# Kernel tuning notes

Measured on AMD Instinct MI355X. Metric: run time of the kernel, lower is better.

The kernel has to match this reference:

```python
import jax, jax.numpy as jnp
import numpy as np
from jax import lax

B, S, F, H, A, C = 256, 128, 128, 512, 512, 128


def _gru_cell(x, h, Wih, Whh, bih, bhh):
    # PyTorch GRU cell: gates ordered (r, z, n)
    gi = x @ Wih.T + bih            # [B, 3H]
    gh = h @ Whh.T + bhh            # [B, 3H]
    ir, iz, inn = jnp.split(gi, 3, axis=-1)
    hr, hz, hn = jnp.split(gh, 3, axis=-1)
    r = jax.nn.sigmoid(ir + hr)
    z = jax.nn.sigmoid(iz + hz)
    n = jnp.tanh(inn + r * hn)
    return (1.0 - z) * n + z * h


def setup_inputs() -> dict:
    key = jax.random.key(0)
    ks = jax.random.split(key, 13)
    def n(k, shape, s=0.05):
        return jax.random.normal(k, shape, dtype=jnp.float32) * s
    return dict(
        x=n(ks[0], (B, S, F), 1.0),
        y=jax.random.randint(ks[1], (B, C), 0, S),
        enc_Wih=n(ks[2], (3 * H, F)), enc_Whh=n(ks[3], (3 * H, H)),
        enc_bih=n(ks[4], (3 * H,)), enc_bhh=n(ks[5], (3 * H,)),
        dec_Wih=n(ks[6], (3 * H, F)), dec_Whh=n(ks[7], (3 * H, H)),
        dec_bih=n(ks[8], (3 * H,)), dec_bhh=n(ks[9], (3 * H,)),
        w1=n(ks[10], (A, H)), w2=n(ks[11], (A, H)), v=n(ks[12], (A,)),
    )


def reference(x, y, enc_Wih, enc_Whh, enc_bih, enc_bhh,
              dec_Wih, dec_Whh, dec_bih, dec_bhh, w1, w2, v):
    b, s, f = x.shape
    c = y.shape[1]
    h0 = jnp.zeros((b, H), x.dtype)

    # ---- encoder GRU over sequence ----
    def enc_step(h, xt):
        h2 = _gru_cell(xt, h, enc_Wih, enc_Whh, enc_bih, enc_bhh)
        return h2, h2
    hT, enc_out = lax.scan(enc_step, h0, jnp.swapaxes(x, 0, 1))  # enc_out [S,B,H]
    enc_out = jnp.swapaxes(enc_out, 0, 1)                        # [B,S,H]

    # w1(enc_out) is loop-invariant: precompute (same math as recomputing per step)
    enc_proj = jnp.einsum('bsh,ah->bsa', enc_out, w1)            # [B,S,A]

    # ---- decoder pointer loop (teacher_force_ratio=0.0 -> always use argmax) ----
    def dec_step(carry, y_i):
        h, dec_in = carry
        h = _gru_cell(dec_in, h, dec_Wih, dec_Whh, dec_bih, dec_bhh)  # [B,H]
        att = jax.nn.relu(enc_proj + (h @ w2.T)[:, None, :])          # [B,S,A]
        prob = jax.nn.softmax(jnp.einsum('bsa,a->bs', att, v), axis=1)  # [B,S]
        # faithful to original: F.cross_entropy applied to probabilities
        logp = jax.nn.log_softmax(prob, axis=1)
        step_loss = -jnp.mean(jnp.take_along_axis(logp, y_i[:, None], axis=1))
        pred = jnp.argmax(prob, axis=1)                               # [B]
        dec_in_next = jnp.take_along_axis(x, pred[:, None, None], axis=1)[:, 0, :]
        return (h, dec_in_next), (pred, step_loss)

    dec_in0 = jnp.zeros((b, f), x.dtype)
    (_, _), (preds, losses) = lax.scan(dec_step, (hT, dec_in0), y.T)
    preds = preds.T                                   # [B, C]
    loss = jnp.sum(losses) / b / c
    return preds, loss
```

## Files before the change

kernel.cpp:

```cpp
#include <hip/hip_runtime.h>
#include <math.h>

#define B_ 256
#define S_ 128
#define F_ 128
#define H_ 512
#define A_ 512
#define C_ 128
#define HSLICE (H_ * B_)

#define DOT4(va, vb) ((va).x*(vb).x + (va).y*(vb).y + (va).z*(vb).z + (va).w*(vb).w)

template<int NH>
__device__ __forceinline__ void acc_chunks(const float* __restrict__ src,
                                           const float* __restrict__ W6k,
                                           int nk, int b, float* __restrict__ acc)
{
    float a0[32], a1[32];
#pragma unroll
    for (int j = 0; j < 32; ++j) a0[j] = src[(size_t)j * B_ + b];
    for (int kc = 0; kc < nk; kc += 32) {
        if (kc + 32 < nk) {
#pragma unroll
            for (int j = 0; j < 32; ++j)
                a1[j] = src[(size_t)(kc + 32 + j) * B_ + b];
        }
        const float* Wr = W6k + (size_t)kc * 6;
#pragma unroll
        for (int j = 0; j < 32; ++j) {
            float av = a0[j];
            acc[0]    = fmaf(av, Wr[j * 6 + 0], acc[0]);
            acc[1]    = fmaf(av, Wr[j * 6 + 1], acc[1]);
            acc[2]    = fmaf(av, Wr[j * 6 + 2], acc[2]);
            acc[3]    = fmaf(av, Wr[j * 6 + 3], acc[3]);
            acc[NH]   = fmaf(av, Wr[j * 6 + 4], acc[NH]);
            acc[NH+1] = fmaf(av, Wr[j * 6 + 5], acc[NH + 1]);
        }
#pragma unroll
        for (int j = 0; j < 32; ++j) a0[j] = a1[j];
    }
}

__device__ __forceinline__ void acc_xrow(const float4* __restrict__ xr,
                                         const float* __restrict__ W6k,
                                         float* __restrict__ acc)
{
    float4 c0[8], c1[8];
#pragma unroll
    for (int j = 0; j < 8; ++j) c0[j] = xr[j];
    for (int q = 0; q < 32; q += 8) {
        if (q + 8 < 32) {
#pragma unroll
            for (int j = 0; j < 8; ++j) c1[j] = xr[q + 8 + j];
        }
#pragma unroll
        for (int j = 0; j < 8; ++j) {
            const float* Wr = W6k + (size_t)((q + j) * 4) * 6;
            float e0 = c0[j].x, e1 = c0[j].y, e2 = c0[j].z, e3 = c0[j].w;
#pragma unroll
            for (int t2 = 0; t2 < 4; ++t2) {
                float av = (t2 == 0) ? e0 : (t2 == 1) ? e1 : (t2 == 2) ? e2 : e3;
                acc[0] = fmaf(av, Wr[t2 * 6 + 0], acc[0]);
                acc[1] = fmaf(av, Wr[t2 * 6 + 1], acc[1]);
                acc[2] = fmaf(av, Wr[t2 * 6 + 2], acc[2]);
                acc[3] = fmaf(av, Wr[t2 * 6 + 3], acc[3]);
                acc[4] = fmaf(av, Wr[t2 * 6 + 4], acc[4]);
                acc[5] = fmaf(av, Wr[t2 * 6 + 5], acc[5]);
            }
        }
#pragma unroll
        for (int j = 0; j < 8; ++j) c0[j] = c1[j];
    }
}

__global__ __launch_bounds__(256)
void prep_all(const float* __restrict__ x,
              const float* __restrict__ eWih, const float* __restrict__ eWhh,
              const float* __restrict__ ebih, const float* __restrict__ ebhh,
              const float* __restrict__ dbih, const float* __restrict__ dbhh,
              float* __restrict__ xT, float* __restrict__ W6e,
              float* __restrict__ bias4e, float* __restrict__ bias4d,
              float* __restrict__ h0T)
{
    int id = blockIdx.x * 256 + threadIdx.x;
    {
        int up = id / 3840;
        int rem = id - up * 3840;
        int k = rem / 6, g = rem - k * 6;
        int row = (g >> 1) * H_ + up * 2 + (g & 1);
        float val;
        if (k < F_) val = eWih[(size_t)row * F_ + k];
        else        val = eWhh[(size_t)row * H_ + (k - F_)];
        W6e[id] = val;
    }
#pragma unroll
    for (int r = 0; r < 5; ++r) {
        int xid = id + r * 983040;
        if (xid < S_ * F_ * B_) {
            int b2 = xid & 255, f = (xid >> 8) & 127, t = xid >> 15;
            xT[xid] = x[(size_t)b2 * (S_ * F_) + (size_t)t * F_ + f];
        }
    }
    if (id < H_ * B_) h0T[id] = 0.f;
    if (id < H_) {
        bias4e[id * 4 + 0] = ebih[id] + ebhh[id];
        bias4e[id * 4 + 1] = ebih[H_ + id] + ebhh[H_ + id];
        bias4e[id * 4 + 2] = ebih[2 * H_ + id];
        bias4e[id * 4 + 3] = ebhh[2 * H_ + id];
        bias4d[id * 4 + 0] = dbih[id] + dbhh[id];
        bias4d[id * 4 + 1] = dbih[H_ + id] + dbhh[H_ + id];
        bias4d[id * 4 + 2] = dbih[2 * H_ + id];
        bias4d[id * 4 + 3] = dbhh[2 * H_ + id];
    }
}

__global__ __launch_bounds__(256)
void prep_dec(const float* __restrict__ dWih, const float* __restrict__ dWhh,
              const float* __restrict__ w2,
              float* __restrict__ W6d, float4* __restrict__ w2q)
{
    int id = blockIdx.x * 256 + threadIdx.x;
    {
        int up = id / 3840;
        int rem = id - up * 3840;
        int k = rem / 6, g = rem - k * 6;
        int row = (g >> 1) * H_ + up * 2 + (g & 1);
        float val;
        if (k < F_) val = dWih[(size_t)row * F_ + k];
        else        val = dWhh[(size_t)row * H_ + (k - F_)];
        W6d[id] = val;
    }
    if (id < 128 * 512) {
        int k4 = id >> 9, a = id & 511;
        const float* s = w2 + (size_t)a * H_ + k4 * 4;
        w2q[id] = make_float4(s[0], s[1], s[2], s[3]);
    }
}

__global__ __launch_bounds__(128)
void gru_step(const float* __restrict__ inT,
              const float* __restrict__ x,
              const int*   __restrict__ pred,
              const float* __restrict__ hinT,
              const float* __restrict__ W6,
              const float* __restrict__ bias4,
              float* __restrict__ houtT,
              float* __restrict__ hB)
{
    __shared__ float accL[64][6];
    const int tid = threadIdx.x;
    const int lane = tid & 63;
    const int kw = tid >> 6;
    const int up = blockIdx.x & 255;
    const int bh = blockIdx.x >> 8;
    const int b = bh * 64 + lane;
    const float* Wb = W6 + (size_t)up * 3840;
    const int u0 = up * 2, u1 = u0 + 1;

    float acc[8];
#pragma unroll
    for (int g = 0; g < 8; ++g) acc[g] = 0.f;

    float hold0 = 0.f, hold1 = 0.f;
    if (kw == 0) {
        hold0 = hinT[(size_t)u0 * B_ + b];
        hold1 = hinT[(size_t)u1 * B_ + b];
        if (inT) {
            acc_chunks<4>(inT, Wb, F_, b, acc);
        } else if (pred) {
            int pb = pred[b];
            const float4* xr = (const float4*)(x + ((size_t)b * S_ + pb) * F_);
            acc_xrow(xr, Wb, acc);
        }
        acc_chunks<6>(hinT, Wb + F_ * 6, 192, b, acc);
    } else {
        acc_chunks<6>(hinT + (size_t)192 * B_, Wb + 320 * 6, 320, b, acc);
    }

    if (kw == 1) {
        accL[lane][0] = acc[0]; accL[lane][1] = acc[1];
        accL[lane][2] = acc[2]; accL[lane][3] = acc[3];
        accL[lane][4] = acc[6]; accL[lane][5] = acc[7];
    }
    __syncthreads();
    if (kw == 0) {
        const float4 bb0 = *(const float4*)(bias4 + u0 * 4);
        const float4 bb1 = *(const float4*)(bias4 + u1 * 4);
        float rr0 = 1.f / (1.f + expf(-(acc[0] + accL[lane][0] + bb0.x)));
        float rr1 = 1.f / (1.f + expf(-(acc[1] + accL[lane][1] + bb1.x)));
        float zz0 = 1.f / (1.f + expf(-(acc[2] + accL[lane][2] + bb0.y)));
        float zz1 = 1.f / (1.f + expf(-(acc[3] + accL[lane][3] + bb1.y)));
        float hn0 = acc[6] + accL[lane][4] + bb0.w;
        float hn1 = acc[7] + accL[lane][5] + bb1.w;
        float nn0 = tanhf(acc[4] + bb0.z + rr0 * hn0);
        float nn1 = tanhf(acc[5] + bb1.z + rr1 * hn1);
        float h0v = (1.f - zz0) * nn0 + zz0 * hold0;
        float h1v = (1.f - zz1) * nn1 + zz1 * hold1;
        houtT[(size_t)u0 * B_ + b] = h0v;
        houtT[(size_t)u1 * B_ + b] = h1v;
        if (hB) {
            hB[(size_t)b * H_ + u0] = h0v;
            hB[(size_t)b * H_ + u1] = h1v;
        }
    }
}

__global__ __launch_bounds__(512)
void w2attn_step(const float* __restrict__ hB,
                 const float4* __restrict__ w2q,
                 const float* __restrict__ v, const int* __restrict__ y,
                 int step, const float* __restrict__ proj,
                 int* __restrict__ predBuf,
                 float* __restrict__ nlogp, float* __restrict__ preds_out)
{
    const int b = blockIdx.x;
    const int tid = threadIdx.x;
    __shared__ float sh[512];
    __shared__ float sq[512];
    __shared__ float sScore[S_], sProb[S_];

    sh[tid] = hB[(size_t)b * H_ + tid];
    __syncthreads();

    {
        float acc = 0.f;
        const float4* wp = w2q + tid;
#pragma unroll 8
        for (int k4 = 0; k4 < 128; ++k4) {
            float4 hv = *(const float4*)&sh[k4 * 4];
            float4 wv4 = wp[(size_t)k4 * 512];
            acc += DOT4(hv, wv4);
        }
        sq[tid] = acc;
    }
    __syncthreads();

    const int wv = tid >> 6, ln = tid & 63;
    float4 q0 = *(const float4*)&sq[ln * 8];
    float4 q1 = *(const float4*)&sq[ln * 8 + 4];
    float4 v0r = *(const float4*)(v + ln * 8);
    float4 v1r = *(const float4*)(v + ln * 8 + 4);
    const float* epb = proj + (size_t)b * (S_ * A_);
    for (int si = 0; si < 16; ++si) {
        int s = si * 8 + wv;
        const float* row = epb + (size_t)s * A_ + ln * 8;
        float4 p0 = *(const float4*)(row);
        float4 p1 = *(const float4*)(row + 4);
        float acc = fmaxf(p0.x + q0.x, 0.f) * v0r.x
                  + fmaxf(p0.y + q0.y, 0.f) * v0r.y
                  + fmaxf(p0.z + q0.z, 0.f) * v0r.z
                  + fmaxf(p0.w + q0.w, 0.f) * v0r.w
                  + fmaxf(p1.x + q1.x, 0.f) * v1r.x
                  + fmaxf(p1.y + q1.y, 0.f) * v1r.y
                  + fmaxf(p1.z + q1.z, 0.f) * v1r.z
                  + fmaxf(p1.w + q1.w, 0.f) * v1r.w;
#pragma unroll
        for (int off = 32; off; off >>= 1) acc += __shfl_down(acc, off);
        if (ln == 0) sScore[s] = acc;
    }
    __syncthreads();

    if (tid < 64) {
        float s0v = sScore[tid], s1v = sScore[tid + 64];
        float m = fmaxf(s0v, s1v);
#pragma unroll
        for (int off = 32; off; off >>= 1) m = fmaxf(m, __shfl_xor(m, off));
        float e0 = expf(s0v - m), e1 = expf(s1v - m);
        float se = e0 + e1;
#pragma unroll
        for (int off = 32; off; off >>= 1) se += __shfl_xor(se, off);
        float p0 = e0 / se, p1 = e1 / se;
        sProb[tid] = p0; sProb[tid + 64] = p1;
        float pm = fmaxf(p0, p1);
#pragma unroll
        for (int off = 32; off; off >>= 1) pm = fmaxf(pm, __shfl_xor(pm, off));
        float t0 = expf(p0 - pm), t1 = expf(p1 - pm);
        float T = t0 + t1;
#pragma unroll
        for (int off = 32; off; off >>= 1) T += __shfl_xor(T, off);
        float bv = p0; int bi2 = tid;
        if (p1 > bv) { bv = p1; bi2 = tid + 64; }
#pragma unroll
        for (int off = 32; off; off >>= 1) {
            float ov = __shfl_xor(bv, off);
            int oi = __shfl_xor(bi2, off);
            if (ov > bv || (ov == bv && oi < bi2)) { bv = ov; bi2 = oi; }
        }
        if (tid == 0) {
            int yy = y[(size_t)b * C_ + step];
            float py = sProb[yy];
            nlogp[(size_t)step * B_ + b] = -(py - pm - logf(T));
            preds_out[(size_t)b * C_ + step] = (float)bi2;
            predBuf[b] = bi2;
        }
    }
}

__global__ __launch_bounds__(256)
void proj_gemm(const float* __restrict__ encT, const float* __restrict__ w1,
               float* __restrict__ proj)
{
    __shared__ float sA[32][128];
    __shared__ float sB[32][132];
    const int tid = threadIdx.x;
    const int s = blockIdx.z;
    const int b0 = blockIdx.y * 128;
    const int a0 = blockIdx.x * 128;
    const int tx = tid & 15, ty = tid >> 4;

    float acc[8][8];
#pragma unroll
    for (int i = 0; i < 8; ++i)
#pragma unroll
        for (int j = 0; j < 8; ++j) acc[i][j] = 0.f;

    const float* Abase = encT + (size_t)s * HSLICE + b0;
    for (int kc = 0; kc < H_; kc += 32) {
#pragma unroll
        for (int p = 0; p < 16; ++p) {
            int idx = tid + p * 256;
            int kj = idx >> 7, bbb = idx & 127;
            sA[kj][bbb] = Abase[(size_t)(kc + kj) * B_ + bbb];
        }
#pragma unroll
        for (int p = 0; p < 16; ++p) {
            int idx = tid + p * 256;
            int aa = idx >> 5, kj = idx & 31;
            sB[kj][aa] = w1[(size_t)(a0 + aa) * H_ + kc + kj];
        }
        __syncthreads();
#pragma unroll
        for (int kj = 0; kj < 32; ++kj) {
            float4 af0 = *(const float4*)&sA[kj][ty * 8];
            float4 af1 = *(const float4*)&sA[kj][ty * 8 + 4];
            float4 bf0 = *(const float4*)&sB[kj][tx * 8];
            float4 bf1 = *(const float4*)&sB[kj][tx * 8 + 4];
            float am[8] = {af0.x, af0.y, af0.z, af0.w, af1.x, af1.y, af1.z, af1.w};
            float bn[8] = {bf0.x, bf0.y, bf0.z, bf0.w, bf1.x, bf1.y, bf1.z, bf1.w};
#pragma unroll
            for (int i = 0; i < 8; ++i)
#pragma unroll
                for (int j = 0; j < 8; ++j)
                    acc[i][j] = fmaf(am[i], bn[j], acc[i][j]);
        }
        __syncthreads();
    }
#pragma unroll
    for (int i = 0; i < 8; ++i) {
        float* dst = proj + ((size_t)(b0 + ty * 8 + i) * S_ + s) * A_ + a0 + tx * 8;
        *(float4*)(dst) = make_float4(acc[i][0], acc[i][1], acc[i][2], acc[i][3]);
        *(float4*)(dst + 4) = make_float4(acc[i][4], acc[i][5], acc[i][6], acc[i][7]);
    }
}

__global__ void final_loss(const float* __restrict__ nlogp, float* __restrict__ out)
{
    __shared__ float part[C_];
    const int i = threadIdx.x;
    float s = 0.f;
    for (int b = 0; b < B_; ++b) s += nlogp[(size_t)i * B_ + b];
    part[i] = s / (float)B_;
    __syncthreads();
    if (i == 0) {
        float t = 0.f;
        for (int k = 0; k < C_; ++k) t += part[k];
        out[0] = t / (float)B_ / (float)C_;
    }
}

extern "C" void kernel_launch(void* const* d_in, const int* in_sizes, int n_in,
                              void* d_out, int out_size, void* d_ws, size_t ws_size,
                              hipStream_t stream)
{
    (void)in_sizes; (void)n_in; (void)out_size; (void)ws_size;
    const float* x    = (const float*)d_in[0];
    const int*   y    = (const int*)d_in[1];
    const float* eWih = (const float*)d_in[2];
    const float* eWhh = (const float*)d_in[3];
    const float* ebih = (const float*)d_in[4];
    const float* ebhh = (const float*)d_in[5];
    const float* dWih = (const float*)d_in[6];
    const float* dWhh = (const float*)d_in[7];
    const float* dbih = (const float*)d_in[8];
    const float* dbhh = (const float*)d_in[9];
    const float* w1   = (const float*)d_in[10];
    const float* w2   = (const float*)d_in[11];
    const float* v    = (const float*)d_in[12];
    float* out = (float*)d_out;

    float* ws = (float*)d_ws;
    float* encT    = ws;
    float* encT127 = ws + (size_t)127 * HSLICE;
    float* projB  = ws + 16777216;
    float* xT     = projB;
    float* W6e    = projB + 4194304;
    float* h0T    = projB + 5177344;
    float* C0     = ws + 33554432;
    float* bias4e = C0;
    float* bias4d = C0 + 2048;
    float* nlogp  = C0 + 4096;
    float* hT0    = C0 + 36864;
    float* hT1    = C0 + 167936;
    float* hB     = C0 + 299008;
    float* w2qf   = C0 + 430080;
    float* W6d    = C0 + 692224;
    int*   predBuf = (int*)(C0 + 1675264);

    prep_all<<<dim3(3840), 256, 0, stream>>>(x, eWih, eWhh, ebih, ebhh,
                                             dbih, dbhh, xT, W6e,
                                             bias4e, bias4d, h0T);

    for (int t = 0; t < S_; ++t) {
        const float* hin = (t == 0) ? h0T : encT + (size_t)(t - 1) * HSLICE;
        gru_step<<<dim3(1024), 128, 0, stream>>>(
            xT + (size_t)t * (F_ * B_), nullptr, nullptr,
            hin, W6e, bias4e, encT + (size_t)t * HSLICE, nullptr);
    }

    proj_gemm<<<dim3(4, 2, 128), 256, 0, stream>>>(encT, w1, projB);

    prep_dec<<<dim3(3840), 256, 0, stream>>>(dWih, dWhh, w2, W6d, (float4*)w2qf);

    float* hb[2] = { hT0, hT1 };
    for (int st = 0; st < C_; ++st) {
        const float* hin = (st == 0) ? encT127 : hb[(st & 1) ^ 1];
        float* hout = hb[st & 1];
        gru_step<<<dim3(1024), 128, 0, stream>>>(
            nullptr, x, (st > 0) ? predBuf : nullptr,
            hin, W6d, bias4d, hout, hB);
        w2attn_step<<<dim3(256), 512, 0, stream>>>(
            hB, (const float4*)w2qf, v, y, st, projB, predBuf, nlogp, out);
    }

    final_loss<<<dim3(1), 128, 0, stream>>>(nlogp, out + (size_t)B_ * C_);
}
```

Baseline: 7.233 ms.

## Fuse decoder GRU, w2 projection and attention into one kernel with group flags

Replaces the per-step pair of decoder kernels (gru_step plus w2attn_step) with a single dec_fused kernel. Inside it, groups of 128 blocks work on 64 batch rows and synchronise through atomic flag counters in global memory between the GRU, h·w2 and attention phases. This removes one launch per decoder step and the hB transpose buffer. It depends on all 128 blocks of a group being co-resident to avoid deadlock, and adds spin-wait overhead and extra global traffic through hw2.

```diff
diff --git a/kernel.cpp b/kernel.cpp
--- a/kernel.cpp
+++ b/kernel.cpp
@@ -10,6 +10,32 @@
 #define HSLICE (H_ * B_)
 
 #define DOT4(va, vb) ((va).x*(vb).x + (va).y*(vb).y + (va).z*(vb).z + (va).w*(vb).w)
+
+__device__ __forceinline__ void stf(float* p, float v) {
+    __hip_atomic_store(p, v, __ATOMIC_RELAXED, __HIP_MEMORY_SCOPE_AGENT);
+}
+__device__ __forceinline__ void sti(int* p, int v) {
+    __hip_atomic_store(p, v, __ATOMIC_RELAXED, __HIP_MEMORY_SCOPE_AGENT);
+}
+__device__ __forceinline__ float ldf_sc(const float* p) {
+    return __hip_atomic_load(p, __ATOMIC_RELAXED, __HIP_MEMORY_SCOPE_AGENT);
+}
+
+__device__ __forceinline__ void group_wait128(const int* __restrict__ flags,
+                                              int gbase, int tid, int target)
+{
+    if (tid < 64) {
+        while (true) {
+            int v0 = __hip_atomic_load(&flags[gbase + tid], __ATOMIC_RELAXED,
+                                       __HIP_MEMORY_SCOPE_AGENT);
+            int v1 = __hip_atomic_load(&flags[gbase + 64 + tid], __ATOMIC_RELAXED,
+                                       __HIP_MEMORY_SCOPE_AGENT);
+            int mn = v0 < v1 ? v0 : v1;
+            if (__all(mn >= target)) break;
+            __builtin_amdgcn_s_sleep(4);
+        }
+    }
+}
 
 template<int NH>
 __device__ __forceinline__ void acc_chunks(const float* __restrict__ src,
@@ -73,6 +99,27 @@
     }
 }
 
+__device__ __forceinline__ void gru_epilogue(const float* __restrict__ acc,
+                                             const float accL[][6], int li,
+                                             const float* __restrict__ bias4,
+                                             int u0, int u1,
+                                             float hold0, float hold1,
+                                             float* __restrict__ houtT, int b)
+{
+    const float4 bb0 = *(const float4*)(bias4 + u0 * 4);
+    const float4 bb1 = *(const float4*)(bias4 + u1 * 4);
+    float rr0 = 1.f / (1.f + expf(-(acc[0] + accL[li][0] + bb0.x)));
+    float rr1 = 1.f / (1.f + expf(-(acc[1] + accL[li][1] + bb1.x)));
+    float zz0 = 1.f / (1.f + expf(-(acc[2] + accL[li][2] + bb0.y)));
+    float zz1 = 1.f / (1.f + expf(-(acc[3] + accL[li][3] + bb1.y)));
+    float hn0 = acc[6] + accL[li][4] + bb0.w;
+    float hn1 = acc[7] + accL[li][5] + bb1.w;
+    float nn0 = tanhf(acc[4] + bb0.z + rr0 * hn0);
+    float nn1 = tanhf(acc[5] + bb1.z + rr1 * hn1);
+    stf(&houtT[(size_t)u0 * B_ + b], (1.f - zz0) * nn0 + zz0 * hold0);
+    stf(&houtT[(size_t)u1 * B_ + b], (1.f - zz1) * nn1 + zz1 * hold1);
+}
+
 __global__ __launch_bounds__(256)
 void prep_all(const float* __restrict__ x,
               const float* __restrict__ eWih, const float* __restrict__ eWhh,
@@ -80,7 +127,7 @@
               const float* __restrict__ dbih, const float* __restrict__ dbhh,
               float* __restrict__ xT, float* __restrict__ W6e,
               float* __restrict__ bias4e, float* __restrict__ bias4d,
-              float* __restrict__ h0T)
+              float* __restrict__ h0T, int* __restrict__ dflags)
 {
     int id = blockIdx.x * 256 + threadIdx.x;
     {
@@ -102,6 +149,7 @@
         }
     }
     if (id < H_ * B_) h0T[id] = 0.f;
+    if (id < 512) dflags[id] = 0;
     if (id < H_) {
         bias4e[id * 4 + 0] = ebih[id] + ebhh[id];
         bias4e[id * 4 + 1] = ebih[H_ + id] + ebhh[H_ + id];
@@ -116,36 +164,25 @@
 
 __global__ __launch_bounds__(256)
 void prep_dec(const float* __restrict__ dWih, const float* __restrict__ dWhh,
-              const float* __restrict__ w2,
-              float* __restrict__ W6d, float4* __restrict__ w2q)
+              float* __restrict__ W6d)
 {
     int id = blockIdx.x * 256 + threadIdx.x;
-    {
-        int up = id / 3840;
-        int rem = id - up * 3840;
-        int k = rem / 6, g = rem - k * 6;
-        int row = (g >> 1) * H_ + up * 2 + (g & 1);
-        float val;
-        if (k < F_) val = dWih[(size_t)row * F_ + k];
-        else        val = dWhh[(size_t)row * H_ + (k - F_)];
-        W6d[id] = val;
-    }
-    if (id < 128 * 512) {
-        int k4 = id >> 9, a = id & 511;
-        const float* s = w2 + (size_t)a * H_ + k4 * 4;
-        w2q[id] = make_float4(s[0], s[1], s[2], s[3]);
-    }
+    int up = id / 3840;
+    int rem = id - up * 3840;
+    int k = rem / 6, g = rem - k * 6;
+    int row = (g >> 1) * H_ + up * 2 + (g & 1);
+    float val;
+    if (k < F_) val = dWih[(size_t)row * F_ + k];
+    else        val = dWhh[(size_t)row * H_ + (k - F_)];
+    W6d[id] = val;
 }
 
 __global__ __launch_bounds__(128)
 void gru_step(const float* __restrict__ inT,
-              const float* __restrict__ x,
-              const int*   __restrict__ pred,
               const float* __restrict__ hinT,
               const float* __restrict__ W6,
               const float* __restrict__ bias4,
-              float* __restrict__ houtT,
-              float* __restrict__ hB)
+              float* __restrict__ houtT)
 {
     __shared__ float accL[64][6];
     const int tid = threadIdx.x;
@@ -165,13 +202,7 @@
     if (kw == 0) {
         hold0 = hinT[(size_t)u0 * B_ + b];
         hold1 = hinT[(size_t)u1 * B_ + b];
-        if (inT) {
-            acc_chunks<4>(inT, Wb, F_, b, acc);
-        } else if (pred) {
-            int pb = pred[b];
-            const float4* xr = (const float4*)(x + ((size_t)b * S_ + pb) * F_);
-            acc_xrow(xr, Wb, acc);
-        }
+        acc_chunks<4>(inT, Wb, F_, b, acc);
         acc_chunks<6>(hinT, Wb + F_ * 6, 192, b, acc);
     } else {
         acc_chunks<6>(hinT + (size_t)192 * B_, Wb + 320 * 6, 320, b, acc);
@@ -194,104 +225,172 @@
         float hn1 = acc[7] + accL[lane][5] + bb1.w;
         float nn0 = tanhf(acc[4] + bb0.z + rr0 * hn0);
         float nn1 = tanhf(acc[5] + bb1.z + rr1 * hn1);
-        float h0v = (1.f - zz0) * nn0 + zz0 * hold0;
-        float h1v = (1.f - zz1) * nn1 + zz1 * hold1;
-        houtT[(size_t)u0 * B_ + b] = h0v;
-        houtT[(size_t)u1 * B_ + b] = h1v;
-        if (hB) {
-            hB[(size_t)b * H_ + u0] = h0v;
-            hB[(size_t)b * H_ + u1] = h1v;
-        }
-    }
-}
-
-__global__ __launch_bounds__(512)
-void w2attn_step(const float* __restrict__ hB,
-                 const float4* __restrict__ w2q,
-                 const float* __restrict__ v, const int* __restrict__ y,
-                 int step, const float* __restrict__ proj,
-                 int* __restrict__ predBuf,
-                 float* __restrict__ nlogp, float* __restrict__ preds_out)
-{
-    const int b = blockIdx.x;
+        houtT[(size_t)u0 * B_ + b] = (1.f - zz0) * nn0 + zz0 * hold0;
+        houtT[(size_t)u1 * B_ + b] = (1.f - zz1) * nn1 + zz1 * hold1;
+    }
+}
+
+__global__ __launch_bounds__(256)
+void dec_fused(const float* __restrict__ x,
+               const int*   __restrict__ y,
+               const float* __restrict__ W6,
+               const float* __restrict__ bias4,
+               const float* __restrict__ w2,
+               const float* __restrict__ v,
+               const float* __restrict__ proj,
+               const float* __restrict__ hinT,
+               float* __restrict__ houtT,
+               float* __restrict__ hw2,
+               int* __restrict__ predBuf,
+               float* __restrict__ nlogp, float* __restrict__ preds_out,
+               int step, int* __restrict__ dflags)
+{
+    __shared__ float accL[2][64][6];
+    __shared__ float sh[512];
+    __shared__ float sScore[S_], sProb[S_];
+
     const int tid = threadIdx.x;
-    __shared__ float sh[512];
-    __shared__ float sq[512];
-    __shared__ float sScore[S_], sProb[S_];
-
-    sh[tid] = hB[(size_t)b * H_ + tid];
+    const int lane = tid & 63;
+    const int wv = __builtin_amdgcn_readfirstlane(tid >> 6);
+    const int bid = blockIdx.x;
+    const int g = bid >> 7;
+    const int j = bid & 127;
+    const int gbase = g * 128;
+
+    {
+        const int up_local = wv & 1;
+        const int kw = wv >> 1;
+        const int upp = j;
+        const int up = upp * 2 + up_local;
+        const int b = g * 64 + lane;
+        const float* Wb = W6 + (size_t)up * 3840;
+        const int u0 = up * 2, u1 = u0 + 1;
+
+        float acc[8];
+#pragma unroll
+        for (int q = 0; q < 8; ++q) acc[q] = 0.f;
+
+        float hold0 = 0.f, hold1 = 0.f;
+        if (kw == 0) {
+            hold0 = hinT[(size_t)u0 * B_ + b];
+            hold1 = hinT[(size_t)u1 * B_ + b];
+            if (step > 0) {
+                int pb = predBuf[b];
+                const float4* xr = (const float4*)(x + ((size_t)b * S_ + pb) * F_);
+                acc_xrow(xr, Wb, acc);
+            }
+            acc_chunks<6>(hinT, Wb + F_ * 6, 192, b, acc);
+        } else {
+            acc_chunks<6>(hinT + (size_t)192 * B_, Wb + 320 * 6, 320, b, acc);
+        }
+
+        if (kw == 1) {
+            accL[up_local][lane][0] = acc[0]; accL[up_local][lane][1] = acc[1];
+            accL[up_local][lane][2] = acc[2]; accL[up_local][lane][3] = acc[3];
+            accL[up_local][lane][4] = acc[6]; accL[up_local][lane][5] = acc[7];
+        }
+        __syncthreads();
+        if (kw == 0)
+            gru_epilogue(acc, accL[up_local], lane, bias4, u0, u1,
+                         hold0, hold1, houtT, b);
+        asm volatile("s_waitcnt vmcnt(0)" ::: "memory");
+        __syncthreads();
+        if (tid == 0) sti(&dflags[bid], 2 * step + 1);
+    }
+
+    group_wait128(dflags, gbase, tid, 2 * step + 1);
     __syncthreads();
-
     {
-        float acc = 0.f;
-        const float4* wp = w2q + tid;
-#pragma unroll 8
-        for (int k4 = 0; k4 < 128; ++k4) {
-            float4 hv = *(const float4*)&sh[k4 * 4];
-            float4 wv4 = wp[(size_t)k4 * 512];
-            acc += DOT4(hv, wv4);
-        }
-        sq[tid] = acc;
-    }
+        const int a = j * 4 + wv;
+        const int b = g * 64 + lane;
+        const float* wrow = w2 + (size_t)a * H_;
+        float accw = 0.f;
+        float c0[16], c1[16];
+#pragma unroll
+        for (int q = 0; q < 16; ++q) c0[q] = houtT[(size_t)q * B_ + b];
+        for (int kc = 0; kc < H_; kc += 16) {
+            if (kc + 16 < H_) {
+#pragma unroll
+                for (int q = 0; q < 16; ++q)
+                    c1[q] = houtT[(size_t)(kc + 16 + q) * B_ + b];
+            }
+#pragma unroll
+            for (int q = 0; q < 16; ++q)
+                accw = fmaf(c0[q], wrow[kc + q], accw);
+#pragma unroll
+            for (int q = 0; q < 16; ++q) c0[q] = c1[q];
+        }
+        stf(&hw2[(size_t)b * A_ + a], accw);
+        asm volatile("s_waitcnt vmcnt(0)" ::: "memory");
+        __syncthreads();
+        if (tid == 0) sti(&dflags[bid], 2 * step + 2);
+    }
+
+    group_wait128(dflags, gbase, tid, 2 * step + 2);
     __syncthreads();
-
-    const int wv = tid >> 6, ln = tid & 63;
-    float4 q0 = *(const float4*)&sq[ln * 8];
-    float4 q1 = *(const float4*)&sq[ln * 8 + 4];
-    float4 v0r = *(const float4*)(v + ln * 8);
-    float4 v1r = *(const float4*)(v + ln * 8 + 4);
-    const float* epb = proj + (size_t)b * (S_ * A_);
-    for (int si = 0; si < 16; ++si) {
-        int s = si * 8 + wv;
-        const float* row = epb + (size_t)s * A_ + ln * 8;
-        float4 p0 = *(const float4*)(row);
-        float4 p1 = *(const float4*)(row + 4);
-        float acc = fmaxf(p0.x + q0.x, 0.f) * v0r.x
-                  + fmaxf(p0.y + q0.y, 0.f) * v0r.y
-                  + fmaxf(p0.z + q0.z, 0.f) * v0r.z
-                  + fmaxf(p0.w + q0.w, 0.f) * v0r.w
-                  + fmaxf(p1.x + q1.x, 0.f) * v1r.x
-                  + fmaxf(p1.y + q1.y, 0.f) * v1r.y
-                  + fmaxf(p1.z + q1.z, 0.f) * v1r.z
-                  + fmaxf(p1.w + q1.w, 0.f) * v1r.w;
-#pragma unroll
-        for (int off = 32; off; off >>= 1) acc += __shfl_down(acc, off);
-        if (ln == 0) sScore[s] = acc;
-    }
-    __syncthreads();
-
-    if (tid < 64) {
-        float s0v = sScore[tid], s1v = sScore[tid + 64];
-        float m = fmaxf(s0v, s1v);
-#pragma unroll
-        for (int off = 32; off; off >>= 1) m = fmaxf(m, __shfl_xor(m, off));
-        float e0 = expf(s0v - m), e1 = expf(s1v - m);
-        float se = e0 + e1;
-#pragma unroll
-        for (int off = 32; off; off >>= 1) se += __shfl_xor(se, off);
-        float p0 = e0 / se, p1 = e1 / se;
-        sProb[tid] = p0; sProb[tid + 64] = p1;
-        float pm = fmaxf(p0, p1);
-#pragma unroll
-        for (int off = 32; off; off >>= 1) pm = fmaxf(pm, __shfl_xor(pm, off));
-        float t0 = expf(p0 - pm), t1 = expf(p1 - pm);
-        float T = t0 + t1;
-#pragma unroll
-        for (int off = 32; off; off >>= 1) T += __shfl_xor(T, off);
-        float bv = p0; int bi2 = tid;
-        if (p1 > bv) { bv = p1; bi2 = tid + 64; }
-#pragma unroll
-        for (int off = 32; off; off >>= 1) {
-            float ov = __shfl_xor(bv, off);
-            int oi = __shfl_xor(bi2, off);
-            if (ov > bv || (ov == bv && oi < bi2)) { bv = ov; bi2 = oi; }
-        }
-        if (tid == 0) {
-            int yy = y[(size_t)b * C_ + step];
-            float py = sProb[yy];
-            nlogp[(size_t)step * B_ + b] = -(py - pm - logf(T));
-            preds_out[(size_t)b * C_ + step] = (float)bi2;
-            predBuf[b] = bi2;
+    if (j < 64) {
+        const int bb = g * 64 + j;
+        sh[tid] = ldf_sc(&hw2[(size_t)bb * A_ + tid]);
+        sh[tid + 256] = ldf_sc(&hw2[(size_t)bb * A_ + tid + 256]);
+        __syncthreads();
+
+        float4 q0 = *(const float4*)&sh[lane * 8];
+        float4 q1 = *(const float4*)&sh[lane * 8 + 4];
+        float4 v0r = *(const float4*)(v + lane * 8);
+        float4 v1r = *(const float4*)(v + lane * 8 + 4);
+        const float* epb = proj + (size_t)bb * (S_ * A_);
+        for (int si = 0; si < 32; ++si) {
+            int s = si * 4 + wv;
+            const float* row = epb + (size_t)s * A_ + lane * 8;
+            float4 p0 = *(const float4*)(row);
+            float4 p1 = *(const float4*)(row + 4);
+            float acc = fmaxf(p0.x + q0.x, 0.f) * v0r.x
+                      + fmaxf(p0.y + q0.y, 0.f) * v0r.y
+                      + fmaxf(p0.z + q0.z, 0.f) * v0r.z
+                      + fmaxf(p0.w + q0.w, 0.f) * v0r.w
+                      + fmaxf(p1.x + q1.x, 0.f) * v1r.x
+                      + fmaxf(p1.y + q1.y, 0.f) * v1r.y
+                      + fmaxf(p1.z + q1.z, 0.f) * v1r.z
+                      + fmaxf(p1.w + q1.w, 0.f) * v1r.w;
+#pragma unroll
+            for (int off = 32; off; off >>= 1) acc += __shfl_down(acc, off);
+            if (lane == 0) sScore[s] = acc;
+        }
+        __syncthreads();
+
+        if (tid < 64) {
+            float s0v = sScore[tid], s1v = sScore[tid + 64];
+            float m = fmaxf(s0v, s1v);
+#pragma unroll
+            for (int off = 32; off; off >>= 1) m = fmaxf(m, __shfl_xor(m, off));
+            float e0 = expf(s0v - m), e1 = expf(s1v - m);
+            float se = e0 + e1;
+#pragma unroll
+            for (int off = 32; off; off >>= 1) se += __shfl_xor(se, off);
+            float p0 = e0 / se, p1 = e1 / se;
+            sProb[tid] = p0; sProb[tid + 64] = p1;
+            float pm = fmaxf(p0, p1);
+#pragma unroll
+            for (int off = 32; off; off >>= 1) pm = fmaxf(pm, __shfl_xor(pm, off));
+            float t0 = expf(p0 - pm), t1 = expf(p1 - pm);
+            float T = t0 + t1;
+#pragma unroll
+            for (int off = 32; off; off >>= 1) T += __shfl_xor(T, off);
+            float bv = p0; int bi2 = tid;
+            if (p1 > bv) { bv = p1; bi2 = tid + 64; }
+#pragma unroll
+            for (int off = 32; off; off >>= 1) {
+                float ov = __shfl_xor(bv, off);
+                int oi = __shfl_xor(bi2, off);
+                if (ov > bv || (ov == bv && oi < bi2)) { bv = ov; bi2 = oi; }
+            }
+            if (tid == 0) {
+                int yy = y[(size_t)bb * C_ + step];
+                float py = sProb[yy];
+                nlogp[(size_t)step * B_ + bb] = -(py - pm - logf(T));
+                preds_out[(size_t)bb * C_ + step] = (float)bi2;
+                predBuf[bb] = bi2;
+            }
         }
     }
 }
@@ -312,7 +411,7 @@
 #pragma unroll
     for (int i = 0; i < 8; ++i)
 #pragma unroll
-        for (int j = 0; j < 8; ++j) acc[i][j] = 0.f;
+        for (int jj = 0; jj < 8; ++jj) acc[i][jj] = 0.f;
 
     const float* Abase = encT + (size_t)s * HSLICE + b0;
     for (int kc = 0; kc < H_; kc += 32) {
@@ -340,8 +439,8 @@
 #pragma unroll
             for (int i = 0; i < 8; ++i)
 #pragma unroll
-                for (int j = 0; j < 8; ++j)
-                    acc[i][j] = fmaf(am[i], bn[j], acc[i][j]);
+                for (int jj = 0; jj < 8; ++jj)
+                    acc[i][jj] = fmaf(am[i], bn[jj], acc[i][jj]);
         }
         __syncthreads();
     }
@@ -401,35 +500,33 @@
     float* nlogp  = C0 + 4096;
     float* hT0    = C0 + 36864;
     float* hT1    = C0 + 167936;
-    float* hB     = C0 + 299008;
-    float* w2qf   = C0 + 430080;
-    float* W6d    = C0 + 692224;
-    int*   predBuf = (int*)(C0 + 1675264);
+    float* hw2    = C0 + 299008;
+    float* W6d    = C0 + 430080;
+    int*   predBuf = (int*)(C0 + 1413120);
+    int*   dflags  = predBuf + 256;
 
     prep_all<<<dim3(3840), 256, 0, stream>>>(x, eWih, eWhh, ebih, ebhh,
                                              dbih, dbhh, xT, W6e,
-                                             bias4e, bias4d, h0T);
+                                             bias4e, bias4d, h0T, dflags);
 
     for (int t = 0; t < S_; ++t) {
         const float* hin = (t == 0) ? h0T : encT + (size_t)(t - 1) * HSLICE;
         gru_step<<<dim3(1024), 128, 0, stream>>>(
-            xT + (size_t)t * (F_ * B_), nullptr, nullptr,
-            hin, W6e, bias4e, encT + (size_t)t * HSLICE, nullptr);
+            xT + (size_t)t * (F_ * B_), hin, W6e, bias4e,
+            encT + (size_t)t * HSLICE);
     }
 
     proj_gemm<<<dim3(4, 2, 128), 256, 0, stream>>>(encT, w1, projB);
 
-    prep_dec<<<dim3(3840), 256, 0, stream>>>(dWih, dWhh, w2, W6d, (float4*)w2qf);
+    prep_dec<<<dim3(3840), 256, 0, stream>>>(dWih, dWhh, W6d);
 
     float* hb[2] = { hT0, hT1 };
     for (int st = 0; st < C_; ++st) {
         const float* hin = (st == 0) ? encT127 : hb[(st & 1) ^ 1];
         float* hout = hb[st & 1];
-        gru_step<<<dim3(1024), 128, 0, stream>>>(
-            nullptr, x, (st > 0) ? predBuf : nullptr,
-            hin, W6d, bias4d, hout, hB);
-        w2attn_step<<<dim3(256), 512, 0, stream>>>(
-            hB, (const float4*)w2qf, v, y, st, projB, predBuf, nlogp, out);
+        dec_fused<<<dim3(512), 256, 0, stream>>>(
+            x, y, W6d, bias4d, w2, v, projB, hin, hout, hw2,
+            predBuf, nlogp, out, st, dflags);
     }
 
     final_loss<<<dim3(1), 128, 0, stream>>>(nlogp, out + (size_t)B_ * C_);
```

Result: slower. 9.890 ms (+36.7%).
